# Kernel tuning notes

Hardware: AMD Instinct MI355X
Metric: run time of the kernel (lower is better)

The kernel has to match this reference:

```python
import jax, jax.numpy as jnp
import numpy as np

B, H, S, DK = 2, 16, 2048, 64

def setup_inputs() -> dict:
    key = jax.random.key(0)
    kq, kk, kv = jax.random.split(key, 3)
    shape = (B, H, S, DK)
    return {
        "multi_head_q": jax.random.normal(kq, shape, dtype=jnp.float32),
        "multi_head_k": jax.random.normal(kk, shape, dtype=jnp.float32),
        "multi_head_v": jax.random.normal(kv, shape, dtype=jnp.float32),
    }

def reference(multi_head_q, multi_head_k, multi_head_v):
    d_k = multi_head_q.shape[-1]
    scale = 1.0 / jnp.sqrt(jnp.asarray(d_k, dtype=multi_head_q.dtype))
    # scores: [B, H, S, S]
    scores = jnp.einsum("bhqd,bhkd->bhqk", multi_head_q, multi_head_k) * scale
    attn = jax.nn.softmax(scores, axis=-1)
    # z: [B, H, S, DK]
    z = jnp.einsum("bhqk,bhkd->bhqd", attn, multi_head_v)
    # transpose heads to [B, S, H, DK] then merge -> [B, S, H*DK]
    b, h, s, d = z.shape
    return jnp.swapaxes(z, 1, 2).reshape(b, s, h * d)
```

## Files before the change

### kernel.cpp

```cpp
#include <hip/hip_runtime.h>
#include <cmath>


#define S_LEN   2048
#define D_HEAD  64
#define NHEADS  16
#define NBH     32
#define TQ      128
#define TK      64
#define NTILE   (S_LEN / TK)
#define HTILE   (NTILE / 2)
#define LDSTR   72
#define TILE_SH 4096

typedef short bfrag8 __attribute__((ext_vector_type(8)));
typedef float f32x4  __attribute__((ext_vector_type(4)));
typedef float f32x16 __attribute__((ext_vector_type(16)));
typedef int   i32x2  __attribute__((ext_vector_type(2)));
typedef int   i32x4  __attribute__((ext_vector_type(4)));

static __device__ __forceinline__ short f2bf(float f) {
  return (short)__builtin_bit_cast(unsigned short, (__bf16)f);
}

static __device__ __forceinline__ int pk2bf(float a, float b) {
  unsigned short lo = __builtin_bit_cast(unsigned short, (__bf16)a);
  unsigned short hi = __builtin_bit_cast(unsigned short, (__bf16)b);
  return (int)lo | ((int)hi << 16);
}

static __device__ __forceinline__ float fexp2(float x) {
#if __has_builtin(__builtin_amdgcn_exp2f)
  return __builtin_amdgcn_exp2f(x);
#else
  return exp2f(x);
#endif
}

static __device__ __forceinline__ void gload_lds16(const short* g, short* l) {
  __builtin_amdgcn_global_load_lds(
      (const __attribute__((address_space(1))) void*)g,
      (__attribute__((address_space(3))) void*)l, 16, 0, 0);
}

__global__ __launch_bounds__(256)
void fa_prep(const float* __restrict__ K, const float* __restrict__ V,
             short* __restrict__ Kt, short* __restrict__ Vt) {
  __shared__ float fl[64][65];

  const int tid = threadIdx.x;
  int id = blockIdx.x;
  const bool isV = id >= NBH * NTILE;
  if (isV) id -= NBH * NTILE;
  const int xcd = id & 7;
  const int s   = id >> 3;
  const int bh  = xcd * 4 + (s >> 5);
  const int t   = s & 31;

  const size_t ibase = ((size_t)bh * S_LEN + t * 64) * D_HEAD;

  if (!isV) {
    short* kt = Kt + (size_t)(bh * NTILE + t) * TILE_SH;
#pragma unroll
    for (int p = 0; p < 2; ++p) {
      int idx = p * 256 + tid;
      int key = idx >> 3, c = idx & 7;
      const float* src = K + ibase + key * 64 + c * 8;
      float4 a = *(const float4*)src;
      float4 b = *(const float4*)(src + 4);
      i32x4 w;
      w[0] = pk2bf(a.x, a.y); w[1] = pk2bf(a.z, a.w);
      w[2] = pk2bf(b.x, b.y); w[3] = pk2bf(b.z, b.w);
      *(i32x4*)(kt + key * 64 + ((c ^ (key & 7)) * 8)) = w;
    }
  } else {
    short* vt = Vt + (size_t)(bh * NTILE + t) * TILE_SH;
#pragma unroll
    for (int i = 0; i < 4; ++i) {
      int e = (i * 256 + tid) * 4;
      int row = e >> 6, col = e & 63;
      float4 v = *(const float4*)(V + ibase + (size_t)row * 64 + col);
      fl[col + 0][row] = v.x;
      fl[col + 1][row] = v.y;
      fl[col + 2][row] = v.z;
      fl[col + 3][row] = v.w;
    }
    __syncthreads();
#pragma unroll
    for (int p = 0; p < 2; ++p) {
      int idx = p * 256 + tid;
      int d = idx >> 3, ck = idx & 7;
      const float* row = &fl[d][ck * 8];
      i32x4 w;
      w[0] = pk2bf(row[0], row[1]); w[1] = pk2bf(row[2], row[3]);
      w[2] = pk2bf(row[4], row[5]); w[3] = pk2bf(row[6], row[7]);
      *(i32x4*)(vt + d * 64 + ((ck ^ (d & 7)) * 8)) = w;
    }
  }
}

__global__ __launch_bounds__(512, 4)
void fa_fwd3(const float* __restrict__ Q, const short* __restrict__ Kt,
             const short* __restrict__ Vt, float* __restrict__ Out) {
  __shared__ short Ksb[2][2][TILE_SH];
  __shared__ short Vsb[2][2][TILE_SH];

  const int tid    = threadIdx.x;
  const int wid    = tid >> 6;
  const int stream = wid >> 2;
  const int qw     = wid & 3;
  const int lane   = tid & 63;
  const int h      = lane >> 5;
  const int c      = lane & 31;
  const int c7     = c & 7;
  const int qb     = 32 * qw;

  const int id   = blockIdx.x;
  const int xcd  = id & 7;
  const int slot = id >> 3;
  const int bh   = xcd * 4 + (slot >> 4);
  const int q0   = (slot & 15) * 128;

  const int t0   = stream * HTILE;

  const float qscale = 0.125f * 1.44269504088896340736f;

  const float* Qg = Q + ((size_t)bh * S_LEN + (q0 + qb + c)) * D_HEAD;
  bfrag8 qf[4];
#pragma unroll
  for (int sl = 0; sl < 4; ++sl) {
    const float* qp = Qg + 16 * sl + 8 * h;
    float4 a = *(const float4*)qp;
    float4 b = *(const float4*)(qp + 4);
    i32x4 w;
    w[0] = pk2bf(a.x * qscale, a.y * qscale);
    w[1] = pk2bf(a.z * qscale, a.w * qscale);
    w[2] = pk2bf(b.x * qscale, b.y * qscale);
    w[3] = pk2bf(b.z * qscale, b.w * qscale);
    qf[sl] = __builtin_bit_cast(bfrag8, w);
  }

  const short* ktb = Kt + (size_t)bh * NTILE * TILE_SH;
  const short* vtb = Vt + (size_t)bh * NTILE * TILE_SH;

  auto stage = [&](int b, int t) {
    const short* ks = ktb + (size_t)t * TILE_SH;
    const short* vs = vtb + (size_t)t * TILE_SH;
#pragma unroll
    for (int n = 0; n < 2; ++n) {
      int ch = (qw * 2 + n) * 512;
      gload_lds16(ks + ch + lane * 8, &Ksb[stream][b][ch]);
      gload_lds16(vs + ch + lane * 8, &Vsb[stream][b][ch]);
    }
  };

  f32x16 acc[2];
#pragma unroll
  for (int m = 0; m < 2; ++m)
#pragma unroll
    for (int i = 0; i < 16; ++i) acc[m][i] = 0.f;

  float lrun = 0.f;

  auto compute = [&](const short* ksb, const short* vsb) {
    f32x16 st[2];
#pragma unroll
    for (int m = 0; m < 2; ++m)
#pragma unroll
      for (int i = 0; i < 16; ++i) st[m][i] = 0.f;

    __builtin_amdgcn_s_setprio(1);
#pragma unroll
    for (int sl = 0; sl < 4; ++sl) {
#pragma unroll
      for (int m2 = 0; m2 < 2; ++m2) {
        bfrag8 af = *(const bfrag8*)
            &ksb[(32 * m2 + c) * 64 + (((2 * sl + h) ^ c7) * 8)];
        st[m2] = __builtin_amdgcn_mfma_f32_32x32x16_bf16(af, qf[sl], st[m2], 0, 0, 0);
      }
    }
    __builtin_amdgcn_s_setprio(0);

    float ls = 0.f;
#pragma unroll
    for (int m2 = 0; m2 < 2; ++m2)
#pragma unroll
      for (int i = 0; i < 16; ++i) {
        st[m2][i] = fexp2(st[m2][i]);
        ls += st[m2][i];
      }
    lrun += ls;

    bfrag8 pf[4];
#pragma unroll
    for (int m2 = 0; m2 < 2; ++m2)
#pragma unroll
      for (int hf = 0; hf < 2; ++hf) {
        const int b0 = 8 * hf;
        int w0 = pk2bf(st[m2][b0 + 0], st[m2][b0 + 1]);
        int w1 = pk2bf(st[m2][b0 + 2], st[m2][b0 + 3]);
        int w2 = pk2bf(st[m2][b0 + 4], st[m2][b0 + 5]);
        int w3 = pk2bf(st[m2][b0 + 6], st[m2][b0 + 7]);
        asm("v_permlane32_swap_b32 %0, %1" : "+v"(w0), "+v"(w2));
        asm("v_permlane32_swap_b32 %0, %1" : "+v"(w1), "+v"(w3));
        i32x4 f; f[0] = w0; f[1] = w1; f[2] = w2; f[3] = w3;
        pf[2 * m2 + hf] = __builtin_bit_cast(bfrag8, f);
      }

    __builtin_amdgcn_s_setprio(1);
#pragma unroll
    for (int sl = 0; sl < 4; ++sl) {
#pragma unroll
      for (int mtd = 0; mtd < 2; ++mtd) {
        bfrag8 av = *(const bfrag8*)
            &vsb[(32 * mtd + c) * 64 + (((2 * sl + h) ^ c7) * 8)];
        acc[mtd] = __builtin_amdgcn_mfma_f32_32x32x16_bf16(av, pf[sl], acc[mtd], 0, 0, 0);
      }
    }
    __builtin_amdgcn_s_setprio(0);
  };

  stage(0, t0);
  for (int t = 0; t < HTILE; t += 2) {
    __syncthreads();
    stage(1, t0 + t + 1);
    compute(Ksb[stream][0], Vsb[stream][0]);
    __syncthreads();
    if (t + 2 < HTILE) stage(0, t0 + t + 2);
    compute(Ksb[stream][1], Vsb[stream][1]);
  }

  float* red = (float*)&Ksb[0][0][0];
  __syncthreads();
  if (stream == 1) {
    const int base = (tid - 256) * 33;
#pragma unroll
    for (int m = 0; m < 2; ++m)
#pragma unroll
      for (int i = 0; i < 16; ++i) red[base + 16 * m + i] = acc[m][i];
    red[base + 32] = lrun;
  }
  __syncthreads();
  if (stream == 0) {
    const int base = tid * 33;
#pragma unroll
    for (int m = 0; m < 2; ++m)
#pragma unroll
      for (int i = 0; i < 16; ++i) acc[m][i] += red[base + 16 * m + i];
    float l = lrun + red[base + 32];
    l += __shfl_xor(l, 32);
    float inv = 1.0f / l;
    const int bb = bh >> 4, hh = bh & 15;
    const int qg = q0 + qb + c;
    float* op = Out + ((size_t)bb * S_LEN + qg) * (NHEADS * D_HEAD) + hh * D_HEAD;
#pragma unroll
    for (int mtd = 0; mtd < 2; ++mtd)
#pragma unroll
      for (int g = 0; g < 4; ++g) {
        float4 o;
        o.x = acc[mtd][4 * g + 0] * inv;
        o.y = acc[mtd][4 * g + 1] * inv;
        o.z = acc[mtd][4 * g + 2] * inv;
        o.w = acc[mtd][4 * g + 3] * inv;
        *(float4*)(op + 32 * mtd + 8 * g + 4 * h) = o;
      }
  }
}

__global__ __launch_bounds__(256, 2)
void fa_fwd(const float* __restrict__ Q, const float* __restrict__ K,
            const float* __restrict__ V, float* __restrict__ Out) {
  __shared__ short Ks [2][TK * LDSTR];
  __shared__ short VsT[2][D_HEAD * LDSTR];
  __shared__ short Psf[TQ * LDSTR];

  const int tid  = threadIdx.x;
  const int wid  = tid >> 6;
  const int lane = tid & 63;
  const int quad = lane >> 4;
  const int r    = lane & 15;
  const int qb   = 32 * wid;

  const int bh = blockIdx.y;
  const int q0 = blockIdx.x * TQ;

  const float* Qg = Q + (size_t)bh * S_LEN * D_HEAD;
  const float* Kg = K + (size_t)bh * S_LEN * D_HEAD;
  const float* Vg = V + (size_t)bh * S_LEN * D_HEAD;

  const float qscale = 0.125f * 1.44269504088896340736f;

  bfrag8 qf[2][2];
#pragma unroll
  for (int nt = 0; nt < 2; ++nt)
#pragma unroll
    for (int ks = 0; ks < 2; ++ks) {
      const float* qp = Qg + (size_t)(q0 + qb + 16 * nt + r) * D_HEAD + 32 * ks + 8 * quad;
      float4 a = *(const float4*)qp;
      float4 b = *(const float4*)(qp + 4);
      i32x4 w;
      w[0] = pk2bf(a.x * qscale, a.y * qscale);
      w[1] = pk2bf(a.z * qscale, a.w * qscale);
      w[2] = pk2bf(b.x * qscale, b.y * qscale);
      w[3] = pk2bf(b.z * qscale, b.w * qscale);
      qf[nt][ks] = __builtin_bit_cast(bfrag8, w);
    }

  float4 kpre[4];
  float  vpre[16];

  auto load_tile = [&](int k0) {
#pragma unroll
    for (int i = 0; i < 4; ++i) {
      int e = (i * 256 + tid) * 4;
      kpre[i] = *(const float4*)(Kg + (size_t)(k0 + (e >> 6)) * D_HEAD + (e & 63));
    }
    const float* vpp = Vg + (size_t)(k0 + wid * 16) * D_HEAD + lane;
#pragma unroll
    for (int j = 0; j < 16; ++j) vpre[j] = vpp[(size_t)j * D_HEAD];
  };

  auto store_tile = [&](short* ksb, short* vsb) {
#pragma unroll
    for (int i = 0; i < 4; ++i) {
      int e = (i * 256 + tid) * 4;
      i32x2 w;
      w[0] = pk2bf(kpre[i].x, kpre[i].y);
      w[1] = pk2bf(kpre[i].z, kpre[i].w);
      *(i32x2*)&ksb[(e >> 6) * LDSTR + (e & 63)] = w;
    }
    i32x4 w0, w1;
#pragma unroll
    for (int j = 0; j < 4; ++j) w0[j] = pk2bf(vpre[2 * j],     vpre[2 * j + 1]);
#pragma unroll
    for (int j = 0; j < 4; ++j) w1[j] = pk2bf(vpre[8 + 2 * j], vpre[9 + 2 * j]);
    *(i32x4*)&vsb[lane * LDSTR + wid * 16]     = w0;
    *(i32x4*)&vsb[lane * LDSTR + wid * 16 + 8] = w1;
  };

  f32x4 acc[4][2];
#pragma unroll
  for (int mt = 0; mt < 4; ++mt)
#pragma unroll
    for (int nt = 0; nt < 2; ++nt)
      acc[mt][nt] = (f32x4){0.f, 0.f, 0.f, 0.f};

  float lrun[2] = {0.f, 0.f};

  auto compute = [&](const short* ksb, const short* vsb) {
    f32x4 st[4][2];
#pragma unroll
    for (int mt = 0; mt < 4; ++mt)
#pragma unroll
      for (int nt = 0; nt < 2; ++nt)
        st[mt][nt] = (f32x4){0.f, 0.f, 0.f, 0.f};
#pragma unroll
    for (int ks = 0; ks < 2; ++ks) {
      bfrag8 af[4];
#pragma unroll
      for (int mt = 0; mt < 4; ++mt)
        af[mt] = *(const bfrag8*)&ksb[(r + 16 * mt) * LDSTR + quad * 8 + 32 * ks];
#pragma unroll
      for (int mt = 0; mt < 4; ++mt)
#pragma unroll
        for (int nt = 0; nt < 2; ++nt)
          st[mt][nt] = __builtin_amdgcn_mfma_f32_16x16x32_bf16(af[mt], qf[nt][ks], st[mt][nt], 0, 0, 0);
    }
#pragma unroll
    for (int nt = 0; nt < 2; ++nt) {
      float ssum = 0.f;
#pragma unroll
      for (int mt = 0; mt < 4; ++mt) {
        float p0 = fexp2(st[mt][nt][0]);
        float p1 = fexp2(st[mt][nt][1]);
        float p2 = fexp2(st[mt][nt][2]);
        float p3 = fexp2(st[mt][nt][3]);
        ssum += (p0 + p1) + (p2 + p3);
        i32x2 w;
        w[0] = pk2bf(p0, p1);
        w[1] = pk2bf(p2, p3);
        *(i32x2*)&Psf[(qb + 16 * nt + r) * LDSTR + 16 * mt + 4 * quad] = w;
      }
      lrun[nt] += ssum;
    }
#pragma unroll
    for (int ks = 0; ks < 2; ++ks) {
      bfrag8 av[4], bp[2];
#pragma unroll
      for (int mt = 0; mt < 4; ++mt)
        av[mt] = *(const bfrag8*)&vsb[(r + 16 * mt) * LDSTR + quad * 8 + 32 * ks];
#pragma unroll
      for (int nt = 0; nt < 2; ++nt)
        bp[nt] = *(const bfrag8*)&Psf[(qb + 16 * nt + r) * LDSTR + quad * 8 + 32 * ks];
#pragma unroll
      for (int mt = 0; mt < 4; ++mt)
#pragma unroll
        for (int nt = 0; nt < 2; ++nt)
          acc[mt][nt] = __builtin_amdgcn_mfma_f32_16x16x32_bf16(av[mt], bp[nt], acc[mt][nt], 0, 0, 0);
    }
  };

  load_tile(0);
  store_tile(Ks[0], VsT[0]);
  load_tile(TK);

  for (int it = 0; it < NTILE; it += 2) {
    __syncthreads();
    compute(Ks[0], VsT[0]);
    store_tile(Ks[1], VsT[1]);
    if (it + 2 < NTILE) load_tile((it + 2) * TK);
    __syncthreads();
    compute(Ks[1], VsT[1]);
    if (it + 2 < NTILE) {
      store_tile(Ks[0], VsT[0]);
      if (it + 3 < NTILE) load_tile((it + 3) * TK);
    }
  }

  const int bb = bh >> 4, hh = bh & 15;
#pragma unroll
  for (int nt = 0; nt < 2; ++nt) {
    float l = lrun[nt];
    l += __shfl_xor(l, 16);
    l += __shfl_xor(l, 32);
    float inv = 1.0f / l;
    int qg = q0 + qb + 16 * nt + r;
    float* op = Out + ((size_t)bb * S_LEN + qg) * (NHEADS * D_HEAD) + hh * D_HEAD;
#pragma unroll
    for (int mt = 0; mt < 4; ++mt) {
      float4 o;
      o.x = acc[mt][nt][0] * inv; o.y = acc[mt][nt][1] * inv;
      o.z = acc[mt][nt][2] * inv; o.w = acc[mt][nt][3] * inv;
      *(float4*)(op + 16 * mt + 4 * quad) = o;
    }
  }
}

extern "C" void kernel_launch(void* const* d_in, const int* in_sizes, int n_in,
                              void* d_out, int out_size, void* d_ws, size_t ws_size,
                              hipStream_t stream) {
  const float* Q = (const float*)d_in[0];
  const float* K = (const float*)d_in[1];
  const float* V = (const float*)d_in[2];
  float* O = (float*)d_out;

  const size_t telems = (size_t)NBH * NTILE * TILE_SH;
  const size_t need   = 2 * telems * sizeof(short);

  if (ws_size >= need) {
    short* Kt = (short*)d_ws;
    short* Vt = Kt + telems;
    fa_prep<<<dim3(2 * NBH * NTILE), 256, 0, stream>>>(K, V, Kt, Vt);
    fa_fwd3<<<dim3(512), 512, 0, stream>>>(Q, Kt, Vt, O);
  } else {
    dim3 grid(S_LEN / TQ, NBH);
    fa_fwd<<<grid, 256, 0, stream>>>(Q, K, V, O);
  }
}
```

Measured before the change: 134.9 us.

## Split key sequence across four wave streams with 32-key tiles

The fused attention kernel now uses 1024-thread blocks in which four groups of waves each process a quarter of the key sequence using 32-key tiles, instead of two groups using 64-key tiles. The prep kernel rewrites V into a 32-key sub-tile layout with a matching swizzle. The partial accumulators are then combined through shared memory in two reduction passes. The aim is more waves in flight per query block, which hides latency better, at the cost of smaller MFMA work per synchronisation, more barriers and a larger final reduction.

```diff
diff --git a/kernel.cpp b/kernel.cpp
--- a/kernel.cpp
+++ b/kernel.cpp
@@ -7,21 +7,19 @@
 #define NHEADS  16
 #define NBH     32
 #define TQ      128
-#define TK      64
+#define TK      32
 #define NTILE   (S_LEN / TK)
-#define HTILE   (NTILE / 2)
+#define NSTREAM 4
+#define HTILE   (NTILE / NSTREAM)
 #define LDSTR   72
-#define TILE_SH 4096
+#define TILE_SH (TK * D_HEAD)
+#define PAIR_SH 4096
 
 typedef short bfrag8 __attribute__((ext_vector_type(8)));
 typedef float f32x4  __attribute__((ext_vector_type(4)));
 typedef float f32x16 __attribute__((ext_vector_type(16)));
 typedef int   i32x2  __attribute__((ext_vector_type(2)));
 typedef int   i32x4  __attribute__((ext_vector_type(4)));
-
-static __device__ __forceinline__ short f2bf(float f) {
-  return (short)__builtin_bit_cast(unsigned short, (__bf16)f);
-}
 
 static __device__ __forceinline__ int pk2bf(float a, float b) {
   unsigned short lo = __builtin_bit_cast(unsigned short, (__bf16)a);
@@ -50,8 +48,8 @@
 
   const int tid = threadIdx.x;
   int id = blockIdx.x;
-  const bool isV = id >= NBH * NTILE;
-  if (isV) id -= NBH * NTILE;
+  const bool isV = id >= NBH * (NTILE / 2);
+  if (isV) id -= NBH * (NTILE / 2);
   const int xcd = id & 7;
   const int s   = id >> 3;
   const int bh  = xcd * 4 + (s >> 5);
@@ -60,7 +58,7 @@
   const size_t ibase = ((size_t)bh * S_LEN + t * 64) * D_HEAD;
 
   if (!isV) {
-    short* kt = Kt + (size_t)(bh * NTILE + t) * TILE_SH;
+    short* kt = Kt + (size_t)(bh * (NTILE / 2) + t) * PAIR_SH;
 #pragma unroll
     for (int p = 0; p < 2; ++p) {
       int idx = p * 256 + tid;
@@ -74,7 +72,7 @@
       *(i32x4*)(kt + key * 64 + ((c ^ (key & 7)) * 8)) = w;
     }
   } else {
-    short* vt = Vt + (size_t)(bh * NTILE + t) * TILE_SH;
+    short* vt = Vt + (size_t)(bh * (NTILE / 2) + t) * PAIR_SH;
 #pragma unroll
     for (int i = 0; i < 4; ++i) {
       int e = (i * 256 + tid) * 4;
@@ -94,16 +92,19 @@
       i32x4 w;
       w[0] = pk2bf(row[0], row[1]); w[1] = pk2bf(row[2], row[3]);
       w[2] = pk2bf(row[4], row[5]); w[3] = pk2bf(row[6], row[7]);
-      *(i32x4*)(vt + d * 64 + ((ck ^ (d & 7)) * 8)) = w;
-    }
-  }
-}
-
-__global__ __launch_bounds__(512, 4)
+      short* dst = vt + (ck >> 2) * TILE_SH + d * 32
+                      + (((ck & 3) ^ ((d >> 1) & 3)) * 8);
+      *(i32x4*)dst = w;
+    }
+  }
+}
+
+__global__ __launch_bounds__(1024, 8)
 void fa_fwd3(const float* __restrict__ Q, const short* __restrict__ Kt,
              const short* __restrict__ Vt, float* __restrict__ Out) {
-  __shared__ short Ksb[2][2][TILE_SH];
-  __shared__ short Vsb[2][2][TILE_SH];
+  __shared__ short SMEM[2 * NSTREAM * 2 * TILE_SH];
+  short* Ks = SMEM;
+  short* Vs = SMEM + NSTREAM * 2 * TILE_SH;
 
   const int tid    = threadIdx.x;
   const int wid    = tid >> 6;
@@ -113,6 +114,7 @@
   const int h      = lane >> 5;
   const int c      = lane & 31;
   const int c7     = c & 7;
+  const int c13    = (c >> 1) & 3;
   const int qb     = 32 * qw;
 
   const int id   = blockIdx.x;
@@ -144,14 +146,14 @@
   const short* vtb = Vt + (size_t)bh * NTILE * TILE_SH;
 
   auto stage = [&](int b, int t) {
-    const short* ks = ktb + (size_t)t * TILE_SH;
-    const short* vs = vtb + (size_t)t * TILE_SH;
-#pragma unroll
-    for (int n = 0; n < 2; ++n) {
-      int ch = (qw * 2 + n) * 512;
-      gload_lds16(ks + ch + lane * 8, &Ksb[stream][b][ch]);
-      gload_lds16(vs + ch + lane * 8, &Vsb[stream][b][ch]);
-    }
+    const int gt = t0 + t;
+    const short* ksrc = ktb + (size_t)gt * TILE_SH;
+    const short* vsrc = vtb + (size_t)gt * TILE_SH;
+    const int ch = qw * 512;
+    short* kdst = Ks + (stream * 2 + b) * TILE_SH + ch;
+    short* vdst = Vs + (stream * 2 + b) * TILE_SH + ch;
+    gload_lds16(ksrc + ch + lane * 8, kdst);
+    gload_lds16(vsrc + ch + lane * 8, vdst);
   };
 
   f32x16 acc[2];
@@ -163,92 +165,98 @@
   float lrun = 0.f;
 
   auto compute = [&](const short* ksb, const short* vsb) {
-    f32x16 st[2];
-#pragma unroll
-    for (int m = 0; m < 2; ++m)
-#pragma unroll
-      for (int i = 0; i < 16; ++i) st[m][i] = 0.f;
+    f32x16 st;
+#pragma unroll
+    for (int i = 0; i < 16; ++i) st[i] = 0.f;
 
     __builtin_amdgcn_s_setprio(1);
 #pragma unroll
     for (int sl = 0; sl < 4; ++sl) {
-#pragma unroll
-      for (int m2 = 0; m2 < 2; ++m2) {
-        bfrag8 af = *(const bfrag8*)
-            &ksb[(32 * m2 + c) * 64 + (((2 * sl + h) ^ c7) * 8)];
-        st[m2] = __builtin_amdgcn_mfma_f32_32x32x16_bf16(af, qf[sl], st[m2], 0, 0, 0);
-      }
+      bfrag8 af = *(const bfrag8*)
+          &ksb[c * 64 + (((2 * sl + h) ^ c7) * 8)];
+      st = __builtin_amdgcn_mfma_f32_32x32x16_bf16(af, qf[sl], st, 0, 0, 0);
     }
     __builtin_amdgcn_s_setprio(0);
 
     float ls = 0.f;
 #pragma unroll
-    for (int m2 = 0; m2 < 2; ++m2)
-#pragma unroll
-      for (int i = 0; i < 16; ++i) {
-        st[m2][i] = fexp2(st[m2][i]);
-        ls += st[m2][i];
-      }
+    for (int i = 0; i < 16; ++i) {
+      st[i] = fexp2(st[i]);
+      ls += st[i];
+    }
     lrun += ls;
 
-    bfrag8 pf[4];
-#pragma unroll
-    for (int m2 = 0; m2 < 2; ++m2)
-#pragma unroll
-      for (int hf = 0; hf < 2; ++hf) {
-        const int b0 = 8 * hf;
-        int w0 = pk2bf(st[m2][b0 + 0], st[m2][b0 + 1]);
-        int w1 = pk2bf(st[m2][b0 + 2], st[m2][b0 + 3]);
-        int w2 = pk2bf(st[m2][b0 + 4], st[m2][b0 + 5]);
-        int w3 = pk2bf(st[m2][b0 + 6], st[m2][b0 + 7]);
-        asm("v_permlane32_swap_b32 %0, %1" : "+v"(w0), "+v"(w2));
-        asm("v_permlane32_swap_b32 %0, %1" : "+v"(w1), "+v"(w3));
-        i32x4 f; f[0] = w0; f[1] = w1; f[2] = w2; f[3] = w3;
-        pf[2 * m2 + hf] = __builtin_bit_cast(bfrag8, f);
-      }
+    bfrag8 pf[2];
+#pragma unroll
+    for (int hf = 0; hf < 2; ++hf) {
+      const int b0 = 8 * hf;
+      int w0 = pk2bf(st[b0 + 0], st[b0 + 1]);
+      int w1 = pk2bf(st[b0 + 2], st[b0 + 3]);
+      int w2 = pk2bf(st[b0 + 4], st[b0 + 5]);
+      int w3 = pk2bf(st[b0 + 6], st[b0 + 7]);
+      asm("v_permlane32_swap_b32 %0, %1" : "+v"(w0), "+v"(w2));
+      asm("v_permlane32_swap_b32 %0, %1" : "+v"(w1), "+v"(w3));
+      i32x4 f; f[0] = w0; f[1] = w1; f[2] = w2; f[3] = w3;
+      pf[hf] = __builtin_bit_cast(bfrag8, f);
+    }
 
     __builtin_amdgcn_s_setprio(1);
 #pragma unroll
-    for (int sl = 0; sl < 4; ++sl) {
+    for (int sl2 = 0; sl2 < 2; ++sl2) {
 #pragma unroll
       for (int mtd = 0; mtd < 2; ++mtd) {
         bfrag8 av = *(const bfrag8*)
-            &vsb[(32 * mtd + c) * 64 + (((2 * sl + h) ^ c7) * 8)];
-        acc[mtd] = __builtin_amdgcn_mfma_f32_32x32x16_bf16(av, pf[sl], acc[mtd], 0, 0, 0);
+            &vsb[(32 * mtd + c) * 32 + (((2 * sl2 + h) ^ c13) * 8)];
+        acc[mtd] = __builtin_amdgcn_mfma_f32_32x32x16_bf16(av, pf[sl2], acc[mtd], 0, 0, 0);
       }
     }
     __builtin_amdgcn_s_setprio(0);
   };
 
-  stage(0, t0);
+  stage(0, 0);
   for (int t = 0; t < HTILE; t += 2) {
     __syncthreads();
-    stage(1, t0 + t + 1);
-    compute(Ksb[stream][0], Vsb[stream][0]);
+    stage(1, t + 1);
+    compute(Ks + (stream * 2 + 0) * TILE_SH, Vs + (stream * 2 + 0) * TILE_SH);
     __syncthreads();
-    if (t + 2 < HTILE) stage(0, t0 + t + 2);
-    compute(Ksb[stream][1], Vsb[stream][1]);
-  }
-
-  float* red = (float*)&Ksb[0][0][0];
+    if (t + 2 < HTILE) stage(0, t + 2);
+    compute(Ks + (stream * 2 + 1) * TILE_SH, Vs + (stream * 2 + 1) * TILE_SH);
+  }
+
+  float* red = (float*)SMEM;
+  const int lt = tid & 255;
   __syncthreads();
-  if (stream == 1) {
-    const int base = (tid - 256) * 33;
-#pragma unroll
-    for (int m = 0; m < 2; ++m)
-#pragma unroll
-      for (int i = 0; i < 16; ++i) red[base + 16 * m + i] = acc[m][i];
-    red[base + 32] = lrun;
+  if (stream > 0) {
+    const int base = ((stream - 1) * 256 + lt) * 17;
+#pragma unroll
+    for (int i = 0; i < 16; ++i) red[base + i] = acc[0][i];
+    red[base + 16] = lrun;
   }
   __syncthreads();
   if (stream == 0) {
-    const int base = tid * 33;
-#pragma unroll
-    for (int m = 0; m < 2; ++m)
-#pragma unroll
-      for (int i = 0; i < 16; ++i) acc[m][i] += red[base + 16 * m + i];
-    float l = lrun + red[base + 32];
-    l += __shfl_xor(l, 32);
+#pragma unroll
+    for (int s = 1; s < NSTREAM; ++s) {
+      const int base = ((s - 1) * 256 + lt) * 17;
+#pragma unroll
+      for (int i = 0; i < 16; ++i) acc[0][i] += red[base + i];
+      lrun += red[base + 16];
+    }
+  }
+  __syncthreads();
+  if (stream > 0) {
+    const int base = ((stream - 1) * 256 + lt) * 17;
+#pragma unroll
+    for (int i = 0; i < 16; ++i) red[base + i] = acc[1][i];
+  }
+  __syncthreads();
+  if (stream == 0) {
+#pragma unroll
+    for (int s = 1; s < NSTREAM; ++s) {
+      const int base = ((s - 1) * 256 + lt) * 17;
+#pragma unroll
+      for (int i = 0; i < 16; ++i) acc[1][i] += red[base + i];
+    }
+    float l = lrun + __shfl_xor(lrun, 32);
     float inv = 1.0f / l;
     const int bb = bh >> 4, hh = bh & 15;
     const int qg = q0 + qb + c;
@@ -270,7 +278,7 @@
 __global__ __launch_bounds__(256, 2)
 void fa_fwd(const float* __restrict__ Q, const float* __restrict__ K,
             const float* __restrict__ V, float* __restrict__ Out) {
-  __shared__ short Ks [2][TK * LDSTR];
+  __shared__ short Ksf [2][64 * LDSTR];
   __shared__ short VsT[2][D_HEAD * LDSTR];
   __shared__ short Psf[TQ * LDSTR];
 
@@ -401,19 +409,19 @@
   };
 
   load_tile(0);
-  store_tile(Ks[0], VsT[0]);
-  load_tile(TK);
-
-  for (int it = 0; it < NTILE; it += 2) {
+  store_tile(Ksf[0], VsT[0]);
+  load_tile(64);
+
+  for (int it = 0; it < S_LEN / 64; it += 2) {
     __syncthreads();
-    compute(Ks[0], VsT[0]);
-    store_tile(Ks[1], VsT[1]);
-    if (it + 2 < NTILE) load_tile((it + 2) * TK);
+    compute(Ksf[0], VsT[0]);
+    store_tile(Ksf[1], VsT[1]);
+    if (it + 2 < S_LEN / 64) load_tile((it + 2) * 64);
     __syncthreads();
-    compute(Ks[1], VsT[1]);
-    if (it + 2 < NTILE) {
-      store_tile(Ks[0], VsT[0]);
-      if (it + 3 < NTILE) load_tile((it + 3) * TK);
+    compute(Ksf[1], VsT[1]);
+    if (it + 2 < S_LEN / 64) {
+      store_tile(Ksf[0], VsT[0]);
+      if (it + 3 < S_LEN / 64) load_tile((it + 3) * 64);
     }
   }
 
@@ -450,8 +458,8 @@
   if (ws_size >= need) {
     short* Kt = (short*)d_ws;
     short* Vt = Kt + telems;
-    fa_prep<<<dim3(2 * NBH * NTILE), 256, 0, stream>>>(K, V, Kt, Vt);
-    fa_fwd3<<<dim3(512), 512, 0, stream>>>(Q, Kt, Vt, O);
+    fa_prep<<<dim3(NBH * NTILE), 256, 0, stream>>>(K, V, Kt, Vt);
+    fa_fwd3<<<dim3(512), 1024, 0, stream>>>(Q, Kt, Vt, O);
   } else {
     dim3 grid(S_LEN / TQ, NBH);
     fa_fwd<<<grid, 256, 0, stream>>>(Q, K, V, O);
```

New measurement: 238.8 us. +77.0%, slower.
